# Performance work log

Hardware: AMD Instinct MI355X
Metric: run time of the kernel (lower is better)

The kernel has to match this reference:

```python
import jax, jax.numpy as jnp
import numpy as np

S, L = 512, 32            # number of sequences, max sequence length
IN_FEATURES = 13824       # 512*3*3 + 1024*3*3 ROI features
HID = 1024                # Head.hidden_dim
LSTM_H = HID // 2         # per-direction hidden size (bidirectional)
N_CLASSES = 4787
BN_EPS = 1e-5


def _make_ragged():
    lengths = (4 + (np.arange(S) % 29)).astype(np.int32)  # 4..32, sum = 9121
    n = int(lengths.sum())
    perm = np.random.RandomState(0).permutation(n).astype(np.int32)
    seq_idx = np.zeros((S, L), dtype=np.int32)
    off = 0
    for i, l in enumerate(lengths):
        seq_idx[i, :l] = perm[off:off + l]
        off += l
    return n, jnp.asarray(seq_idx), jnp.asarray(lengths)


def setup_inputs() -> dict:
    n, seq_idx, lengths = _make_ragged()
    key = jax.random.key(0)
    ks = jax.random.split(key, 16)
    w = lambda k, shp, s=0.02: (jax.random.normal(k, shp, dtype=jnp.float32) * s)
    return {
        "x": jax.random.normal(ks[0], (n, IN_FEATURES), dtype=jnp.float32),
        "fc1_w": w(ks[1], (HID, IN_FEATURES)),
        "fc1_b": w(ks[2], (HID,)),
        "bn_gamma": jnp.ones((HID,), jnp.float32),
        "bn_beta": jnp.zeros((HID,), jnp.float32),
        "fc2_w": w(ks[3], (N_CLASSES, HID)),
        "fc2_b": w(ks[4], (N_CLASSES,)),
        "w_ih_f": w(ks[5], (4 * LSTM_H, HID)),
        "w_hh_f": w(ks[6], (4 * LSTM_H, LSTM_H)),
        "b_ih_f": w(ks[7], (4 * LSTM_H,)),
        "b_hh_f": w(ks[8], (4 * LSTM_H,)),
        "w_ih_b": w(ks[9], (4 * LSTM_H, HID)),
        "w_hh_b": w(ks[10], (4 * LSTM_H, LSTM_H)),
        "b_ih_b": w(ks[11], (4 * LSTM_H,)),
        "b_hh_b": w(ks[12], (4 * LSTM_H,)),
        "seq_idx": seq_idx,
        "lengths": lengths,
    }


def _lstm_scan(seq_x, w_ih, w_hh, b_ih, b_hh):
    # seq_x: [S, L, HID] -> outputs [S, L, LSTM_H]; PyTorch gate order i,f,g,o
    s = seq_x.shape[0]
    h0 = jnp.zeros((s, LSTM_H), seq_x.dtype)
    c0 = jnp.zeros((s, LSTM_H), seq_x.dtype)
    x_gates = jnp.einsum('slh,gh->slg', seq_x, w_ih) + b_ih + b_hh  # precompute input gates

    def step(carry, xg):
        h, c = carry
        g = xg + h @ w_hh.T
        i, f, gg, o = jnp.split(g, 4, axis=-1)
        c = jax.nn.sigmoid(f) * c + jax.nn.sigmoid(i) * jnp.tanh(gg)
        h = jax.nn.sigmoid(o) * jnp.tanh(c)
        return (h, c), h

    _, hs = jax.lax.scan(step, (h0, c0), x_gates.transpose(1, 0, 2))  # [L, S, H]
    return hs.transpose(1, 0, 2)


def reference(x, fc1_w, fc1_b, bn_gamma, bn_beta, fc2_w, fc2_b,
              w_ih_f, w_hh_f, b_ih_f, b_hh_f,
              w_ih_b, w_hh_b, b_ih_b, b_hh_b,
              seq_idx, lengths):
    n = x.shape[0]
    # Head: fc1 -> relu -> BatchNorm1d (training-mode batch stats)
    h = jax.nn.relu(x @ fc1_w.T + fc1_b)
    mean = h.mean(axis=0)
    var = jnp.mean((h - mean) ** 2, axis=0)
    feats = (h - mean) * jax.lax.rsqrt(var + BN_EPS) * bn_gamma + bn_beta  # [N, HID]

    # ragged gather into packed [S, L, HID]
    mask = jnp.arange(L)[None, :] < lengths[:, None]          # [S, L]
    gidx = jnp.where(mask, seq_idx, 0)
    seq_x = feats[gidx] * mask[:, :, None]                    # zero padded slots

    # forward direction (padding at tail: harmless to causal scan)
    hf = _lstm_scan(seq_x, w_ih_f, w_hh_f, b_ih_f, b_hh_f)
    # backward direction: reverse each sequence within its valid length
    rev = jnp.clip(lengths[:, None] - 1 - jnp.arange(L)[None, :], 0, L - 1)  # [S, L]
    seq_rev = jnp.take_along_axis(seq_x, rev[:, :, None], axis=1)
    hb_rev = _lstm_scan(seq_rev, w_ih_b, w_hh_b, b_ih_b, b_hh_b)
    hb = jnp.take_along_axis(hb_rev, rev[:, :, None], axis=1)  # un-reverse (involution on valid region)

    out = jnp.concatenate([hf, hb], axis=-1)                   # [S, L, HID]

    # scatter back to flat roi order; padded slots dropped out-of-bounds
    sidx = jnp.where(mask, seq_idx, n).reshape(-1)
    lstm_feats = jnp.zeros((n, HID), feats.dtype).at[sidx].set(
        out.reshape(-1, HID), mode='drop')

    logits = lstm_feats @ fc2_w.T + fc2_b                      # apply_fc_out
    return logits
```

## Files before the change

kernel.cpp:

```cpp
#include <hip/hip_runtime.h>

typedef short short8v __attribute__((ext_vector_type(8)));
typedef float f32x4 __attribute__((ext_vector_type(4)));
typedef _Float16 h4v __attribute__((ext_vector_type(4)));

__device__ __forceinline__ unsigned short f2bf(float f){
  unsigned int u = __float_as_uint(f);
  u += 0x7fffu + ((u >> 16) & 1u);
  return (unsigned short)(u >> 16);
}
__device__ __forceinline__ float bf2f(unsigned short h){
  return __uint_as_float(((unsigned int)h) << 16);
}
union H2F { unsigned short u; _Float16 h; };
__device__ __forceinline__ float fp16f(unsigned short b){ H2F t; t.u = b; return (float)t.h; }

typedef __attribute__((address_space(1))) const unsigned int gu32;
typedef __attribute__((address_space(3))) unsigned int lu32;
__device__ __forceinline__ void gl16(const void* g, void* l){
  __builtin_amdgcn_global_load_lds((gu32*)g, (lu32*)l, 16, 0, 0);
}

template<int EPI>
__global__ __launch_bounds__(512, 2)
void gemm256(const unsigned short* __restrict__ A, const unsigned short* __restrict__ B,
             void* __restrict__ Cout, int M, int N, int K, int lda, int ldb, int ldc,
             const float* __restrict__ bias)
{
  __shared__ __align__(16) unsigned short As[2 * 2 * 256 * 32];
  __shared__ __align__(16) unsigned short Bs[2 * 2 * 256 * 32];

  const int tid = threadIdx.x;
  const int gx = gridDim.x;
  const int nwg = gx * gridDim.y;
  int dd = blockIdx.y * gx + blockIdx.x;
  int q8 = nwg >> 3, r8 = nwg & 7, xc = dd & 7, t8 = dd >> 3;
  int Lid = (xc < r8 ? xc * (q8 + 1) : r8 * (q8 + 1) + (xc - r8) * q8) + t8;
  const int bcol = (Lid % gx) * 256;
  const int brow = (Lid / gx) * 256;

  const int l = tid & 63, w = tid >> 6;
  const int wr = w >> 2;
  const int wn = w & 3;
  const int r16 = l & 15, kg = l >> 4;
  const int swz = (r16 >> 1) & 3;
  const int srow4 = l >> 2, sblk = l & 3;
  const int scol = (sblk ^ ((l >> 3) & 3)) * 8;

  const int kz = blockIdx.z * K;
  const unsigned short* Ag = A + (size_t)(brow + w * 32 + srow4) * lda + kz + scol;
  const unsigned short* Bg = B + (size_t)(bcol + w * 32 + srow4) * ldb + kz + scol;
  unsigned short* Asd = As + w * 1024;
  unsigned short* Bsd = Bs + w * 1024;

#define STA(buf, kh, kt) do { \
    gl16(Ag + (size_t)(kt) * 64 + (kh) * 32, Asd + (buf) * 16384 + (kh) * 8192); \
    gl16(Ag + (size_t)(kt) * 64 + (kh) * 32 + (size_t)16 * lda, Asd + (buf) * 16384 + (kh) * 8192 + 512); \
  } while (0)
#define STB(buf, kh, kt) do { \
    gl16(Bg + (size_t)(kt) * 64 + (kh) * 32, Bsd + (buf) * 16384 + (kh) * 8192); \
    gl16(Bg + (size_t)(kt) * 64 + (kh) * 32 + (size_t)16 * ldb, Bsd + (buf) * 16384 + (kh) * 8192 + 512); \
  } while (0)

  const unsigned short* Ard = As + (wr * 128 + r16) * 32 + ((kg ^ swz) * 8);
  const unsigned short* Brd = Bs + (wn * 64 + r16) * 32 + ((kg ^ swz) * 8);

  f32x4 acc[8][4];
  #pragma unroll
  for (int m = 0; m < 8; m++)
    #pragma unroll
    for (int nn = 0; nn < 4; nn++) { f32x4 z = {0.f, 0.f, 0.f, 0.f}; acc[m][nn] = z; }

  short8v af[4], bfr[4];

#define LDA4(c, kk, mq) { \
    _Pragma("unroll") for (int i = 0; i < 4; i++) \
      af[i] = *(const short8v*)(Ard + (c) * 16384 + (kk) * 8192 + ((mq) * 4 + i) * 512); }
#define LDB4(c, kk) { \
    _Pragma("unroll") for (int nn = 0; nn < 4; nn++) \
      bfr[nn] = *(const short8v*)(Brd + (c) * 16384 + (kk) * 8192 + nn * 512); }
#define MFMAQ(mq) { \
    __builtin_amdgcn_s_setprio(1); \
    _Pragma("unroll") for (int i = 0; i < 4; i++) { \
      _Pragma("unroll") for (int nn = 0; nn < 4; nn++) \
        acc[(mq) * 4 + i][nn] = __builtin_amdgcn_mfma_f32_16x16x32_bf16(af[i], bfr[nn], acc[(mq) * 4 + i][nn], 0, 0, 0); \
    } \
    __builtin_amdgcn_s_setprio(0); }

  const int nk = K >> 6;
  STA(0, 0, 0); STB(0, 0, 0); STA(0, 1, 0); STB(0, 1, 0);
  asm volatile("s_waitcnt vmcnt(4)" ::: "memory");
  __builtin_amdgcn_s_barrier();
  __builtin_amdgcn_sched_barrier(0);

  for (int j = 0; j < nk; j++) {
    const int c = j & 1, nb = c ^ 1;
    const bool pf = (j + 1 < nk);
    LDB4(c, 0); LDA4(c, 0, 0);
    if (pf) STA(nb, 0, j + 1);
    __builtin_amdgcn_s_barrier();
    MFMAQ(0);
    __builtin_amdgcn_s_barrier();
    LDA4(c, 0, 1);
    if (pf) STB(nb, 0, j + 1);
    __builtin_amdgcn_s_barrier();
    MFMAQ(1);
    if (pf) asm volatile("s_waitcnt vmcnt(4)" ::: "memory");
    else    asm volatile("s_waitcnt vmcnt(0)" ::: "memory");
    __builtin_amdgcn_s_barrier();
    __builtin_amdgcn_sched_barrier(0);
    LDB4(c, 1); LDA4(c, 1, 0);
    if (pf) STA(nb, 1, j + 1);
    __builtin_amdgcn_s_barrier();
    MFMAQ(0);
    __builtin_amdgcn_s_barrier();
    LDA4(c, 1, 1);
    if (pf) STB(nb, 1, j + 1);
    __builtin_amdgcn_s_barrier();
    MFMAQ(1);
    if (pf) asm volatile("s_waitcnt vmcnt(4)" ::: "memory");
    __builtin_amdgcn_s_barrier();
    __builtin_amdgcn_sched_barrier(0);
  }
#undef STA
#undef STB

  #pragma unroll
  for (int m = 0; m < 8; m++) {
    const int row0 = brow + wr * 128 + m * 16 + kg * 4;
    #pragma unroll
    for (int nn = 0; nn < 4; nn++) {
      const int col = bcol + wn * 64 + nn * 16 + r16;
      if (col < N) {
        const float bv = bias[col];
        #pragma unroll
        for (int rr = 0; rr < 4; rr++) {
          const int row = row0 + rr;
          if (row < M) {
            float val = acc[m][nn][rr] + bv;
            if (EPI == 3) {
              int dL = col >> 11, rc = col & 2047;
              int cg = rc >> 6, g = (rc >> 4) & 3, u = rc & 15;
              int pc = (dL << 11) + (((cg << 4) + u) << 2) + g;
              ((_Float16*)Cout)[(size_t)row * ldc + pc] = (_Float16)val;
            } else {
              ((float*)Cout)[(size_t)row * ldc + col] = val;
            }
          }
        }
      }
    }
  }
}

__global__ __launch_bounds__(512, 2)
void gemm256fA(const float* __restrict__ A, const unsigned short* __restrict__ B,
               _Float16* __restrict__ Cout, int M, int N, int K, int lda, int ldb, int ldc,
               int nvalid)
{
  __shared__ __align__(16) unsigned short As[2 * 2 * 256 * 32];
  __shared__ __align__(16) unsigned short Bs[2 * 2 * 256 * 32];

  const int tid = threadIdx.x;
  const int gx = gridDim.x;
  const int nwg = gx * gridDim.y;
  int dd = blockIdx.y * gx + blockIdx.x;
  int q8 = nwg >> 3, r8 = nwg & 7, xc = dd & 7, t8 = dd >> 3;
  int Lid = (xc < r8 ? xc * (q8 + 1) : r8 * (q8 + 1) + (xc - r8) * q8) + t8;
  const int bcol = (Lid % gx) * 256;
  const int brow = (Lid / gx) * 256;

  const int l = tid & 63, w = tid >> 6;
  const int wr = w >> 2;
  const int wn = w & 3;
  const int r16 = l & 15, kg = l >> 4;
  const int swz = (r16 >> 1) & 3;
  const int srow4 = l >> 2, sblk = l & 3;
  const int scol = (sblk ^ ((l >> 3) & 3)) * 8;

  const int kz = blockIdx.z * K;
  const unsigned short* Bg = B + (size_t)(bcol + w * 32 + srow4) * ldb + kz + scol;
  unsigned short* Bsd = Bs + w * 1024;

#define STB(buf, kh, kt) do { \
    gl16(Bg + (size_t)(kt) * 64 + (kh) * 32, Bsd + (buf) * 16384 + (kh) * 8192); \
    gl16(Bg + (size_t)(kt) * 64 + (kh) * 32 + (size_t)16 * ldb, Bsd + (buf) * 16384 + (kh) * 8192 + 512); \
  } while (0)

  const int rsel8 = l >> 3;
  const int g8 = l & 7;
  unsigned long long abase[4];
  int dstA[4];
  #pragma unroll
  for (int q = 0; q < 4; q++) {
    int row_local = w * 32 + q * 8 + rsel8;
    int rowA = brow + row_local;
    if (rowA >= nvalid) rowA = nvalid - 1;
    abase[q] = (unsigned long long)(A + (size_t)rowA * lda + kz + g8 * 8);
    int kh = g8 >> 2, gA = g8 & 3, swi = (row_local >> 1) & 3;
    dstA[q] = kh * 8192 + row_local * 32 + ((gA ^ swi) * 8);
  }

  const unsigned short* Ard = As + (wr * 128 + r16) * 32 + ((kg ^ swz) * 8);
  const unsigned short* Brd = Bs + (wn * 64 + r16) * 32 + ((kg ^ swz) * 8);

  f32x4 acc[8][4];
  #pragma unroll
  for (int m = 0; m < 8; m++)
    #pragma unroll
    for (int nn = 0; nn < 4; nn++) { f32x4 z = {0.f, 0.f, 0.f, 0.f}; acc[m][nn] = z; }

  short8v af[4], bfr[4];
  f32x4 ar[4][2];

#define ALOAD(kt) { \
    _Pragma("unroll") for (int q = 0; q < 4; q++) { \
      unsigned long long aq = abase[q] + (unsigned long long)(kt) * 256; \
      asm volatile("global_load_dwordx4 %0, %1, off" : "=v"(ar[q][0]) : "v"(aq) : "memory"); \
      asm volatile("global_load_dwordx4 %0, %1, off offset:16" : "=v"(ar[q][1]) : "v"(aq) : "memory"); \
    } }
#define AWRITE(buf) { \
    _Pragma("unroll") for (int q = 0; q < 4; q++) { \
      unsigned int d0_, d1_, d2_, d3_; \
      asm("v_cvt_pk_bf16_f32 %0, %1, %2" : "=v"(d0_) : "v"(ar[q][0][0]), "v"(ar[q][0][1])); \
      asm("v_cvt_pk_bf16_f32 %0, %1, %2" : "=v"(d1_) : "v"(ar[q][0][2]), "v"(ar[q][0][3])); \
      asm("v_cvt_pk_bf16_f32 %0, %1, %2" : "=v"(d2_) : "v"(ar[q][1][0]), "v"(ar[q][1][1])); \
      asm("v_cvt_pk_bf16_f32 %0, %1, %2" : "=v"(d3_) : "v"(ar[q][1][2]), "v"(ar[q][1][3])); \
      uint4 pv_; pv_.x = d0_; pv_.y = d1_; pv_.z = d2_; pv_.w = d3_; \
      *(uint4*)(As + (buf) * 16384 + dstA[q]) = pv_; \
    } }

  const int nk = K >> 6;
  ALOAD(0);
  STB(0, 0, 0); STB(0, 1, 0);
  asm volatile("s_waitcnt vmcnt(4)" ::: "memory");
  __builtin_amdgcn_sched_barrier(0);
  AWRITE(0);
  asm volatile("s_waitcnt vmcnt(0) lgkmcnt(0)" ::: "memory");
  __builtin_amdgcn_s_barrier();
  __builtin_amdgcn_sched_barrier(0);

#define LDA4(c, kk, mq) { \
    _Pragma("unroll") for (int i = 0; i < 4; i++) \
      af[i] = *(const short8v*)(Ard + (c) * 16384 + (kk) * 8192 + ((mq) * 4 + i) * 512); }
#define LDB4(c, kk) { \
    _Pragma("unroll") for (int nn = 0; nn < 4; nn++) \
      bfr[nn] = *(const short8v*)(Brd + (c) * 16384 + (kk) * 8192 + nn * 512); }
#define MFMAQ(mq) { \
    __builtin_amdgcn_s_setprio(1); \
    _Pragma("unroll") for (int i = 0; i < 4; i++) { \
      _Pragma("unroll") for (int nn = 0; nn < 4; nn++) \
        acc[(mq) * 4 + i][nn] = __builtin_amdgcn_mfma_f32_16x16x32_bf16(af[i], bfr[nn], acc[(mq) * 4 + i][nn], 0, 0, 0); \
    } \
    __builtin_amdgcn_s_setprio(0); }

  for (int j = 0; j < nk; j++) {
    const int c = j & 1, nb = c ^ 1;
    const bool pf = (j + 1 < nk);
    LDB4(c, 0); LDA4(c, 0, 0);
    if (pf) ALOAD(j + 1);
    __builtin_amdgcn_s_barrier();
    MFMAQ(0);
    __builtin_amdgcn_s_barrier();
    LDA4(c, 0, 1);
    if (pf) { STB(nb, 0, j + 1); STB(nb, 1, j + 1); }
    __builtin_amdgcn_s_barrier();
    MFMAQ(1);
    __builtin_amdgcn_s_barrier();
    __builtin_amdgcn_sched_barrier(0);
    LDB4(c, 1); LDA4(c, 1, 0);
    if (pf) {
      asm volatile("s_waitcnt vmcnt(4)" ::: "memory");
      __builtin_amdgcn_sched_barrier(0);
      AWRITE(nb);
    }
    __builtin_amdgcn_s_barrier();
    MFMAQ(0);
    __builtin_amdgcn_s_barrier();
    LDA4(c, 1, 1);
    __builtin_amdgcn_s_barrier();
    MFMAQ(1);
    asm volatile("s_waitcnt vmcnt(0) lgkmcnt(0)" ::: "memory");
    __builtin_amdgcn_s_barrier();
    __builtin_amdgcn_sched_barrier(0);
  }
#undef STB
#undef ALOAD
#undef AWRITE
#undef LDA4
#undef LDB4
#undef MFMAQ

  #pragma unroll
  for (int m = 0; m < 8; m++) {
    const int row0 = brow + wr * 128 + m * 16 + kg * 4;
    #pragma unroll
    for (int nn = 0; nn < 4; nn++) {
      const int col = bcol + wn * 64 + nn * 16 + r16;
      if (col < N) {
        #pragma unroll
        for (int rr = 0; rr < 4; rr++) {
          const int row = row0 + rr;
          if (row < M)
            Cout[(size_t)blockIdx.z * M * ldc + (size_t)row * ldc + col] = (_Float16)(acc[m][nn][rr]);
        }
      }
    }
  }
}

__global__ __launch_bounds__(256) void fc1_reduce(const _Float16* __restrict__ P, const float* __restrict__ bias,
                                                  unsigned short* __restrict__ h, float* __restrict__ part,
                                                  int n, int mpad) {
  int b = blockIdx.x, tid = threadIdx.x;
  int c0 = tid * 4;
  float4 bsv = *(const float4*)(bias + c0);
  float s[4] = {0,0,0,0}, qq[4] = {0,0,0,0};
  int rbeg = b * 32;
  for (int r = rbeg; r < rbeg + 32; r++) {
    h4v a0 = *(const h4v*)(P + (size_t)r * 1024 + c0);
    h4v a1 = *(const h4v*)(P + ((size_t)mpad + r) * 1024 + c0);
    h4v a2 = *(const h4v*)(P + ((size_t)2 * mpad + r) * 1024 + c0);
    float v0 = fmaxf((float)a0[0] + (float)a1[0] + (float)a2[0] + bsv.x, 0.f);
    float v1 = fmaxf((float)a0[1] + (float)a1[1] + (float)a2[1] + bsv.y, 0.f);
    float v2 = fmaxf((float)a0[2] + (float)a1[2] + (float)a2[2] + bsv.z, 0.f);
    float v3 = fmaxf((float)a0[3] + (float)a1[3] + (float)a2[3] + bsv.w, 0.f);
    if (r < n) {
      s[0] += v0; qq[0] += v0 * v0;
      s[1] += v1; qq[1] += v1 * v1;
      s[2] += v2; qq[2] += v2 * v2;
      s[3] += v3; qq[3] += v3 * v3;
    }
    *(ushort4*)(h + (size_t)r * 1024 + c0) = make_ushort4(f2bf(v0), f2bf(v1), f2bf(v2), f2bf(v3));
  }
  float* pp = part + (size_t)b * 2048;
  #pragma unroll
  for (int k = 0; k < 4; k++) { pp[(c0 + k) * 2] = s[k]; pp[(c0 + k) * 2 + 1] = qq[k]; }
}

__global__ __launch_bounds__(256, 1)
void lstm_persist(const unsigned short* __restrict__ whhc, const unsigned short* __restrict__ bcp,
                  const _Float16* __restrict__ G,
                  const int* __restrict__ gf, const int* __restrict__ gb, const int* __restrict__ sb,
                  unsigned short* __restrict__ hst,
                  unsigned short* __restrict__ lfeat, int* __restrict__ flags)
{
  __shared__ __align__(16) unsigned short Bsh[128 * 512];
  const int tid = threadIdx.x;
  const int l = tid & 63, w = tid >> 6;
  const int b = blockIdx.x;
  const int grp = b & 15;
  const int c = b >> 4;
  const int d = grp >> 3;
  const int rowbase = d * 512 + (grp & 7) * 64;
  const int r16 = l & 15, kg = l >> 4;
  const int swzl = (r16 & 7) * 8;
  const int hu0 = c * 32 + r16;

  const unsigned short* Bsrc = whhc + ((size_t)(d * 2048 + c * 128)) * 512;
  #pragma unroll
  for (int i = 0; i < 32; i++) {
    int rr = w * 32 + i;
    gl16(Bsrc + (size_t)rr * 512 + ((l * 8) ^ ((rr & 7) * 8)), Bsh + rr * 512);
  }
  asm volatile("s_waitcnt vmcnt(0)");
  __syncthreads();

  float creg[2][4];
  #pragma unroll
  for (int m = 0; m < 2; m++)
    #pragma unroll
    for (int rr = 0; rr < 4; rr++) creg[m][rr] = 0.f;

  const size_t stbase = (size_t)(((grp * 4 + w) * 16 + c) * 4 + (r16 >> 3)) * 128 + (size_t)kg * 32 + (r16 & 7);
  const size_t ldbase = ((size_t)(grp * 64 + w * 16) * 1024) + (size_t)l * 16;

  for (int t = 0; t < 32; t++) {
    ushort4 gv[2][4];
    int scv[4];
    #pragma unroll
    for (int rr = 0; rr < 4; rr++) {
      int row = rowbase + w * 16 + kg * 4 + rr;
      int sq = row & 511;
      int gi = d ? gb[sq * 32 + t] : gf[sq * 32 + t];
      const unsigned short* src = (gi >= 0)
          ? (const unsigned short*)G + ((size_t)gi * 4096 + (d << 11))
          : bcp + (d << 11);
      gv[0][rr] = *(const ushort4*)(src + hu0 * 4);
      gv[1][rr] = *(const ushort4*)(src + (hu0 + 16) * 4);
      scv[rr] = d ? sb[sq * 32 + t] : gi;
    }

    if (t > 0) {
      while (true) {
        int fv = 0x7fffffff;
        if (l < 16)
          fv = __hip_atomic_load(flags + ((grp * 16 + l) << 5), __ATOMIC_RELAXED, __HIP_MEMORY_SCOPE_AGENT);
        if (__all(fv >= t)) break;
        __builtin_amdgcn_s_sleep(1);
      }
    }
    asm volatile("" ::: "memory");

    const unsigned short* hp = hst + (size_t)(t & 1) * 524288;
    unsigned short* hn = hst + (size_t)((t + 1) & 1) * 524288;

    short8v av[16];
    {
      unsigned long long a64 = (unsigned long long)((const char*)hp + ldbase);
      #pragma unroll
      for (int kq = 0; kq < 4; kq++) {
        unsigned long long aq = a64 + (unsigned long long)kq * 4096;
        asm volatile("global_load_dwordx4 %0, %1, off offset:0 sc0 sc1"
                     : "=v"(av[kq * 4 + 0]) : "v"(aq) : "memory");
        asm volatile("global_load_dwordx4 %0, %1, off offset:1024 sc0 sc1"
                     : "=v"(av[kq * 4 + 1]) : "v"(aq) : "memory");
        asm volatile("global_load_dwordx4 %0, %1, off offset:2048 sc0 sc1"
                     : "=v"(av[kq * 4 + 2]) : "v"(aq) : "memory");
        asm volatile("global_load_dwordx4 %0, %1, off offset:3072 sc0 sc1"
                     : "=v"(av[kq * 4 + 3]) : "v"(aq) : "memory");
      }
    }
    asm volatile("s_waitcnt vmcnt(0)" ::: "memory");

    f32x4 acc[8];
    #pragma unroll
    for (int nn = 0; nn < 8; nn++) { f32x4 z = {0.f, 0.f, 0.f, 0.f}; acc[nn] = z; }

    #pragma unroll
    for (int kc = 0; kc < 8; kc++) {
      short8v bv[8][2];
      #pragma unroll
      for (int nn = 0; nn < 8; nn++)
        #pragma unroll
        for (int kk = 0; kk < 2; kk++)
          bv[nn][kk] = *(const short8v*)(Bsh + (nn * 16 + r16) * 512 + ((kc * 64 + kk * 32 + kg * 8) ^ swzl));
      #pragma unroll
      for (int kk = 0; kk < 2; kk++)
        #pragma unroll
        for (int nn = 0; nn < 8; nn++)
          acc[nn] = __builtin_amdgcn_mfma_f32_16x16x32_bf16(av[kc * 2 + kk], bv[nn][kk], acc[nn], 0, 0, 0);
    }

    unsigned long long ha = (unsigned long long)((char*)hn + stbase * 2);
    #pragma unroll
    for (int cgl = 0; cgl < 2; cgl++) {
      const int hu = hu0 + cgl * 16;
      #pragma unroll
      for (int reg = 0; reg < 4; reg++) {
        float g_i = acc[cgl * 4 + 0][reg] + fp16f(gv[cgl][reg].x);
        float g_f = acc[cgl * 4 + 1][reg] + fp16f(gv[cgl][reg].y);
        float g_g = acc[cgl * 4 + 2][reg] + fp16f(gv[cgl][reg].z);
        float g_o = acc[cgl * 4 + 3][reg] + fp16f(gv[cgl][reg].w);
        float si = 1.f / (1.f + __expf(-g_i));
        float sf = 1.f / (1.f + __expf(-g_f));
        float so = 1.f / (1.f + __expf(-g_o));
        float cn = sf * creg[cgl][reg] + si * tanhf(g_g);
        float hnv = so * tanhf(cn);
        creg[cgl][reg] = cn;
        unsigned int hb = f2bf(hnv);
        if (cgl == 0) {
          if (reg == 0) asm volatile("global_store_short %0, %1, off offset:0 sc0 sc1" :: "v"(ha), "v"(hb) : "memory");
          if (reg == 1) asm volatile("global_store_short %0, %1, off offset:16 sc0 sc1" :: "v"(ha), "v"(hb) : "memory");
          if (reg == 2) asm volatile("global_store_short %0, %1, off offset:32 sc0 sc1" :: "v"(ha), "v"(hb) : "memory");
          if (reg == 3) asm volatile("global_store_short %0, %1, off offset:48 sc0 sc1" :: "v"(ha), "v"(hb) : "memory");
        } else {
          if (reg == 0) asm volatile("global_store_short %0, %1, off offset:512 sc0 sc1" :: "v"(ha), "v"(hb) : "memory");
          if (reg == 1) asm volatile("global_store_short %0, %1, off offset:528 sc0 sc1" :: "v"(ha), "v"(hb) : "memory");
          if (reg == 2) asm volatile("global_store_short %0, %1, off offset:544 sc0 sc1" :: "v"(ha), "v"(hb) : "memory");
          if (reg == 3) asm volatile("global_store_short %0, %1, off offset:560 sc0 sc1" :: "v"(ha), "v"(hb) : "memory");
        }
        int sc = scv[reg];
        if (sc >= 0) lfeat[(size_t)sc * 1024 + d * 512 + hu] = f2bf(hnv);
      }
    }

    __syncthreads();
    if (t < 31 && tid == 0)
      __hip_atomic_store(flags + ((grp * 16 + c) << 5), t + 1, __ATOMIC_RELAXED, __HIP_MEMORY_SCOPE_AGENT);
  }
}

__global__ __launch_bounds__(256) void conv_bf16(const float* __restrict__ src, unsigned short* __restrict__ dst,
                                                 size_t nvalid, size_t total) {
  size_t stride = (size_t)gridDim.x * 2048;
  for (size_t i = ((size_t)blockIdx.x * 256 + threadIdx.x) * 8; i < total; i += stride) {
    unsigned short o[8];
    if (i + 8 <= nvalid) {
      float4 a = *(const float4*)(src + i);
      float4 b = *(const float4*)(src + i + 4);
      o[0] = f2bf(a.x); o[1] = f2bf(a.y); o[2] = f2bf(a.z); o[3] = f2bf(a.w);
      o[4] = f2bf(b.x); o[5] = f2bf(b.y); o[6] = f2bf(b.z); o[7] = f2bf(b.w);
    } else {
      #pragma unroll
      for (int j = 0; j < 8; j++) o[j] = (i + j < nvalid) ? f2bf(src[i + j]) : (unsigned short)0;
    }
    *(ushort4*)(dst + i) = make_ushort4(o[0], o[1], o[2], o[3]);
    *(ushort4*)(dst + i + 4) = make_ushort4(o[4], o[5], o[6], o[7]);
  }
}

__global__ __launch_bounds__(256) void bn_final(const float* __restrict__ part, const float* __restrict__ gamma,
                                                const float* __restrict__ beta, float* __restrict__ scale,
                                                float* __restrict__ shift, int M, int nb) {
  int c = blockIdx.x * 256 + threadIdx.x;
  float s = 0.f, q = 0.f;
  for (int b = 0; b < nb; b++) { s += part[(size_t)b * 2048 + c * 2]; q += part[(size_t)b * 2048 + c * 2 + 1]; }
  float mean = s / (float)M;
  float var = q / (float)M - mean * mean;
  float sc = gamma[c] * rsqrtf(var + 1e-5f);
  scale[c] = sc; shift[c] = beta[c] - mean * sc;
}

__global__ __launch_bounds__(256) void prep_tables(const int* __restrict__ seq_idx, const int* __restrict__ lengths,
                                                   int* __restrict__ gf, int* __restrict__ gb, int* __restrict__ sb) {
  int idx = blockIdx.x * 256 + threadIdx.x;
  if (idx < 512 * 32) {
    int s = idx >> 5, t = idx & 31;
    int len = lengths[s];
    gf[idx] = (t < len) ? seq_idx[idx] : -1;
    int rb = len - 1 - t;
    gb[idx] = seq_idx[(s << 5) + (rb < 0 ? 0 : rb)];
    sb[idx] = (t < len) ? seq_idx[(s << 5) + (len - 1 - t)] : -1;
  }
}

__global__ __launch_bounds__(256) void build_wih(const float* __restrict__ wf, const float* __restrict__ wb,
                                                 const float* __restrict__ bihf, const float* __restrict__ bhhf,
                                                 const float* __restrict__ bihb, const float* __restrict__ bhhb,
                                                 const float* __restrict__ scale, const float* __restrict__ shift,
                                                 unsigned short* __restrict__ wcdst, float* __restrict__ bc,
                                                 _Float16* __restrict__ bcp) {
  int orow = blockIdx.x * 4 + (threadIdx.x >> 6);
  int l = threadIdx.x & 63;
  int dir = orow >> 11, j = orow & 2047;
  int cc = j >> 6, jj = j & 63, g = jj >> 4, u = jj & 15;
  int srow = g * 512 + cc * 16 + u;
  const float* src = (dir ? wb : wf) + (size_t)srow * 1024;
  unsigned short* dst = wcdst + (size_t)orow * 1024;
  float sacc = 0.f;
  #pragma unroll
  for (int jv = 0; jv < 16; jv++) {
    int k = l + jv * 64;
    float v = src[k];
    sacc += shift[k] * v;
    dst[k] = f2bf(v * scale[k]);
  }
  #pragma unroll
  for (int o2 = 32; o2 > 0; o2 >>= 1) sacc += __shfl_down(sacc, o2);
  if (l == 0) {
    float bb = (dir ? (bihb[srow] + bhhb[srow]) : (bihf[srow] + bhhf[srow])) + sacc;
    bc[orow] = bb;
    int pc = (dir << 11) + (((cc << 4) + u) << 2) + g;
    bcp[pc] = (_Float16)bb;
  }
}

__global__ __launch_bounds__(256) void build_whh(const float* __restrict__ wf, const float* __restrict__ wb,
                                                 unsigned short* __restrict__ o) {
  int cidx = blockIdx.x * 256 + threadIdx.x;
  if (cidx < 4096 * 64) {
    int orow = cidx >> 6, k0 = (cidx & 63) * 8;
    int dir = orow >> 11, j = orow & 2047;
    int cc = j >> 7, L = j & 127;
    int cgl = L >> 6, g = (L >> 4) & 3, u = L & 15;
    int hunit = cc * 32 + cgl * 16 + u;
    const float* src = (dir ? wb : wf) + (size_t)(g * 512 + hunit) * 512 + k0;
    unsigned short* dst = o + (size_t)orow * 512 + k0;
    float4 a = *(const float4*)(src);
    float4 bq = *(const float4*)(src + 4);
    dst[0] = f2bf(a.x); dst[1] = f2bf(a.y); dst[2] = f2bf(a.z); dst[3] = f2bf(a.w);
    dst[4] = f2bf(bq.x); dst[5] = f2bf(bq.y); dst[6] = f2bf(bq.z); dst[7] = f2bf(bq.w);
  }
}

extern "C" void kernel_launch(void* const* d_in, const int* in_sizes, int n_in,
                              void* d_out, int out_size, void* d_ws, size_t ws_size,
                              hipStream_t stream) {
  const float* x     = (const float*)d_in[0];
  const float* fc1w  = (const float*)d_in[1];
  const float* fc1b  = (const float*)d_in[2];
  const float* gamma = (const float*)d_in[3];
  const float* beta  = (const float*)d_in[4];
  const float* fc2w  = (const float*)d_in[5];
  const float* fc2b  = (const float*)d_in[6];
  const float* wihf  = (const float*)d_in[7];
  const float* whhf  = (const float*)d_in[8];
  const float* bihf  = (const float*)d_in[9];
  const float* bhhf  = (const float*)d_in[10];
  const float* wihb  = (const float*)d_in[11];
  const float* whhb  = (const float*)d_in[12];
  const float* bihb  = (const float*)d_in[13];
  const float* bhhb  = (const float*)d_in[14];
  const int* seq_idx = (const int*)d_in[15];
  const int* lengths = (const int*)d_in[16];
  float* out = (float*)d_out;

  const int n = in_sizes[0] / 13824;
  const int mt = (n + 255) / 256;
  const int mpad = mt * 256;

  char* ws = (char*)d_ws;
  size_t off = 0;
  auto alloc = [&](size_t bytes) -> void* {
    void* p = ws + off; off += (bytes + 255) & ~(size_t)255; return p;
  };
  unsigned short* w1_h = (unsigned short*)alloc((size_t)1024 * 13824 * 2);
  unsigned short* w2_h = (unsigned short*)alloc((size_t)4864 * 1024 * 2);
  unsigned short* h    = (unsigned short*)alloc((size_t)mpad * 1024 * 2);
  _Float16*       G    = (_Float16*)alloc((size_t)mpad * 4096 * 2);
  unsigned short* wihc = (unsigned short*)alloc((size_t)4096 * 1024 * 2);
  unsigned short* whhc = (unsigned short*)alloc((size_t)4096 * 512 * 2);
  float* bias_c = (float*)alloc(4096 * 4);
  _Float16* bias_p = (_Float16*)alloc(4096 * 2);
  unsigned short* lfeat  = (unsigned short*)alloc((size_t)mpad * 1024 * 2);
  unsigned short* hstate = (unsigned short*)alloc((size_t)2 * 1024 * 512 * 2);
  float* part   = (float*)alloc((size_t)(mpad / 32) * 2048 * 4);
  float* scale  = (float*)alloc(1024 * 4);
  float* shift  = (float*)alloc(1024 * 4);
  int* gf  = (int*)alloc(16384 * 4);
  int* gb  = (int*)alloc(16384 * 4);
  int* sb  = (int*)alloc(16384 * 4);
  int* flags = (int*)alloc(256 * 32 * 4);

  _Float16* P16 = (_Float16*)G;

  dim3 blk(256);
  dim3 blk5(512);

  conv_bf16<<<1024, blk, 0, stream>>>(fc1w, w1_h, (size_t)1024 * 13824, (size_t)1024 * 13824);
  conv_bf16<<<256, blk, 0, stream>>>(fc2w, w2_h, (size_t)4787 * 1024, (size_t)4864 * 1024);
  build_whh<<<1024, blk, 0, stream>>>(whhf, whhb, whhc);
  prep_tables<<<64, blk, 0, stream>>>(seq_idx, lengths, gf, gb, sb);
  hipMemsetAsync(hstate, 0, (size_t)2 * 1024 * 512 * 2, stream);
  hipMemsetAsync(flags, 0, 256 * 32 * 4, stream);

  gemm256fA<<<dim3(4, mt, 3), blk5, 0, stream>>>(
      x, w1_h, P16, mpad, 1024, 4608, 13824, 13824, 1024, n);

  fc1_reduce<<<mpad / 32, blk, 0, stream>>>(P16, fc1b, h, part, n, mpad);
  bn_final<<<4, blk, 0, stream>>>(part, gamma, beta, scale, shift, n, mpad / 32);
  build_wih<<<1024, blk, 0, stream>>>(wihf, wihb, bihf, bhhf, bihb, bhhb, scale, shift, wihc, bias_c, bias_p);

  gemm256<3><<<dim3(16, mt), blk5, 0, stream>>>(
      h, wihc, G, n, 4096, 1024, 1024, 1024, 4096, bias_c);

  lstm_persist<<<256, blk, 0, stream>>>(whhc, (const unsigned short*)bias_p, G, gf, gb, sb,
                                        hstate, lfeat, flags);

  gemm256<0><<<dim3(19, mt), blk5, 0, stream>>>(
      lfeat, w2_h, out, n, 4787, 1024, 1024, 1024, 4787, fc2b);
}
```

Baseline: 1.091 ms.

## Shrink fc1 split-K GEMM tile to 128x128 with simpler pipeline and higher occupancy

Replaces the 256x256-tile fc1 GEMM (fp32 A converted to bf16 on the fly, split-K by 3) with a 128x128-tile variant. It uses a 64-wide K row with XOR swizzle, fewer barriers per iteration, and launch bounds allowing 4 blocks per CU. The grid grows to 8 x mpad/128 x 3, giving more workgroups for the 256 CUs. In exchange, each workgroup reuses data less, so traffic to global/L2 for the fp32 A matrix and the weights roughly doubles.

```diff
diff --git a/kernel.cpp b/kernel.cpp
--- a/kernel.cpp
+++ b/kernel.cpp
@@ -124,6 +124,9 @@
   }
 #undef STA
 #undef STB
+#undef LDA4
+#undef LDB4
+#undef MFMAQ
 
   #pragma unroll
   for (int m = 0; m < 8; m++) {
@@ -153,13 +156,13 @@
   }
 }
 
-__global__ __launch_bounds__(512, 2)
-void gemm256fA(const float* __restrict__ A, const unsigned short* __restrict__ B,
+__global__ __launch_bounds__(512, 4)
+void gemm128fA(const float* __restrict__ A, const unsigned short* __restrict__ B,
                _Float16* __restrict__ Cout, int M, int N, int K, int lda, int ldb, int ldc,
                int nvalid)
 {
-  __shared__ __align__(16) unsigned short As[2 * 2 * 256 * 32];
-  __shared__ __align__(16) unsigned short Bs[2 * 2 * 256 * 32];
+  __shared__ __align__(16) unsigned short As[2 * 128 * 64];
+  __shared__ __align__(16) unsigned short Bs[2 * 128 * 64];
 
   const int tid = threadIdx.x;
   const int gx = gridDim.x;
@@ -167,136 +170,115 @@
   int dd = blockIdx.y * gx + blockIdx.x;
   int q8 = nwg >> 3, r8 = nwg & 7, xc = dd & 7, t8 = dd >> 3;
   int Lid = (xc < r8 ? xc * (q8 + 1) : r8 * (q8 + 1) + (xc - r8) * q8) + t8;
-  const int bcol = (Lid % gx) * 256;
-  const int brow = (Lid / gx) * 256;
+  const int bcol = (Lid % gx) * 128;
+  const int brow = (Lid / gx) * 128;
 
   const int l = tid & 63, w = tid >> 6;
   const int wr = w >> 2;
   const int wn = w & 3;
   const int r16 = l & 15, kg = l >> 4;
-  const int swz = (r16 >> 1) & 3;
-  const int srow4 = l >> 2, sblk = l & 3;
-  const int scol = (sblk ^ ((l >> 3) & 3)) * 8;
+  const int swzl = (r16 & 7) * 8;
+  const int srow = l >> 3, sg = l & 7;
+  const int stg_off = (sg ^ srow) * 8;
 
   const int kz = blockIdx.z * K;
-  const unsigned short* Bg = B + (size_t)(bcol + w * 32 + srow4) * ldb + kz + scol;
-  unsigned short* Bsd = Bs + w * 1024;
-
-#define STB(buf, kh, kt) do { \
-    gl16(Bg + (size_t)(kt) * 64 + (kh) * 32, Bsd + (buf) * 16384 + (kh) * 8192); \
-    gl16(Bg + (size_t)(kt) * 64 + (kh) * 32 + (size_t)16 * ldb, Bsd + (buf) * 16384 + (kh) * 8192 + 512); \
+  const unsigned short* Bg = B + (size_t)bcol * ldb + kz + stg_off;
+
+#define STBK(buf, kt) do { \
+    gl16(Bg + (size_t)((w * 2 + 0) * 8 + srow) * ldb + (size_t)(kt) * 64, Bs + (buf) * 8192 + (w * 2 + 0) * 512); \
+    gl16(Bg + (size_t)((w * 2 + 1) * 8 + srow) * ldb + (size_t)(kt) * 64, Bs + (buf) * 8192 + (w * 2 + 1) * 512); \
   } while (0)
 
-  const int rsel8 = l >> 3;
-  const int g8 = l & 7;
-  unsigned long long abase[4];
-  int dstA[4];
-  #pragma unroll
-  for (int q = 0; q < 4; q++) {
-    int row_local = w * 32 + q * 8 + rsel8;
+  unsigned long long abase[2];
+  int dstA[2];
+  #pragma unroll
+  for (int q = 0; q < 2; q++) {
+    int row_local = w * 16 + q * 8 + srow;
     int rowA = brow + row_local;
     if (rowA >= nvalid) rowA = nvalid - 1;
-    abase[q] = (unsigned long long)(A + (size_t)rowA * lda + kz + g8 * 8);
-    int kh = g8 >> 2, gA = g8 & 3, swi = (row_local >> 1) & 3;
-    dstA[q] = kh * 8192 + row_local * 32 + ((gA ^ swi) * 8);
-  }
-
-  const unsigned short* Ard = As + (wr * 128 + r16) * 32 + ((kg ^ swz) * 8);
-  const unsigned short* Brd = Bs + (wn * 64 + r16) * 32 + ((kg ^ swz) * 8);
-
-  f32x4 acc[8][4];
-  #pragma unroll
-  for (int m = 0; m < 8; m++)
-    #pragma unroll
-    for (int nn = 0; nn < 4; nn++) { f32x4 z = {0.f, 0.f, 0.f, 0.f}; acc[m][nn] = z; }
-
-  short8v af[4], bfr[4];
-  f32x4 ar[4][2];
+    abase[q] = (unsigned long long)(A + (size_t)rowA * lda + kz + sg * 8);
+    dstA[q] = row_local * 64 + ((sg ^ srow) * 8);
+  }
+
+  const unsigned short* Ard = As + (wr * 64 + r16) * 64;
+  const unsigned short* Brd = Bs + (wn * 32 + r16) * 64;
+
+  f32x4 acc[4][2];
+  #pragma unroll
+  for (int m = 0; m < 4; m++)
+    #pragma unroll
+    for (int nn = 0; nn < 2; nn++) { f32x4 z = {0.f, 0.f, 0.f, 0.f}; acc[m][nn] = z; }
+
+  short8v af[4], bfr[2];
+  f32x4 ar[2][2];
 
 #define ALOAD(kt) { \
-    _Pragma("unroll") for (int q = 0; q < 4; q++) { \
+    _Pragma("unroll") for (int q = 0; q < 2; q++) { \
       unsigned long long aq = abase[q] + (unsigned long long)(kt) * 256; \
       asm volatile("global_load_dwordx4 %0, %1, off" : "=v"(ar[q][0]) : "v"(aq) : "memory"); \
       asm volatile("global_load_dwordx4 %0, %1, off offset:16" : "=v"(ar[q][1]) : "v"(aq) : "memory"); \
     } }
 #define AWRITE(buf) { \
-    _Pragma("unroll") for (int q = 0; q < 4; q++) { \
+    _Pragma("unroll") for (int q = 0; q < 2; q++) { \
       unsigned int d0_, d1_, d2_, d3_; \
       asm("v_cvt_pk_bf16_f32 %0, %1, %2" : "=v"(d0_) : "v"(ar[q][0][0]), "v"(ar[q][0][1])); \
       asm("v_cvt_pk_bf16_f32 %0, %1, %2" : "=v"(d1_) : "v"(ar[q][0][2]), "v"(ar[q][0][3])); \
       asm("v_cvt_pk_bf16_f32 %0, %1, %2" : "=v"(d2_) : "v"(ar[q][1][0]), "v"(ar[q][1][1])); \
       asm("v_cvt_pk_bf16_f32 %0, %1, %2" : "=v"(d3_) : "v"(ar[q][1][2]), "v"(ar[q][1][3])); \
       uint4 pv_; pv_.x = d0_; pv_.y = d1_; pv_.z = d2_; pv_.w = d3_; \
-      *(uint4*)(As + (buf) * 16384 + dstA[q]) = pv_; \
+      *(uint4*)(As + (buf) * 8192 + dstA[q]) = pv_; \
     } }
+#define LDAB(c, kk) { \
+    _Pragma("unroll") for (int i = 0; i < 4; i++) \
+      af[i] = *(const short8v*)(Ard + (c) * 8192 + i * 1024 + (((kk) * 32 + kg * 8) ^ swzl)); \
+    _Pragma("unroll") for (int nn = 0; nn < 2; nn++) \
+      bfr[nn] = *(const short8v*)(Brd + (c) * 8192 + nn * 1024 + (((kk) * 32 + kg * 8) ^ swzl)); }
+#define MFMA8() { \
+    __builtin_amdgcn_s_setprio(1); \
+    _Pragma("unroll") for (int i = 0; i < 4; i++) \
+      _Pragma("unroll") for (int nn = 0; nn < 2; nn++) \
+        acc[i][nn] = __builtin_amdgcn_mfma_f32_16x16x32_bf16(af[i], bfr[nn], acc[i][nn], 0, 0, 0); \
+    __builtin_amdgcn_s_setprio(0); }
 
   const int nk = K >> 6;
   ALOAD(0);
-  STB(0, 0, 0); STB(0, 1, 0);
-  asm volatile("s_waitcnt vmcnt(4)" ::: "memory");
+  STBK(0, 0);
+  asm volatile("s_waitcnt vmcnt(2)" ::: "memory");
   __builtin_amdgcn_sched_barrier(0);
   AWRITE(0);
   asm volatile("s_waitcnt vmcnt(0) lgkmcnt(0)" ::: "memory");
   __builtin_amdgcn_s_barrier();
   __builtin_amdgcn_sched_barrier(0);
 
-#define LDA4(c, kk, mq) { \
-    _Pragma("unroll") for (int i = 0; i < 4; i++) \
-      af[i] = *(const short8v*)(Ard + (c) * 16384 + (kk) * 8192 + ((mq) * 4 + i) * 512); }
-#define LDB4(c, kk) { \
-    _Pragma("unroll") for (int nn = 0; nn < 4; nn++) \
-      bfr[nn] = *(const short8v*)(Brd + (c) * 16384 + (kk) * 8192 + nn * 512); }
-#define MFMAQ(mq) { \
-    __builtin_amdgcn_s_setprio(1); \
-    _Pragma("unroll") for (int i = 0; i < 4; i++) { \
-      _Pragma("unroll") for (int nn = 0; nn < 4; nn++) \
-        acc[(mq) * 4 + i][nn] = __builtin_amdgcn_mfma_f32_16x16x32_bf16(af[i], bfr[nn], acc[(mq) * 4 + i][nn], 0, 0, 0); \
-    } \
-    __builtin_amdgcn_s_setprio(0); }
-
   for (int j = 0; j < nk; j++) {
     const int c = j & 1, nb = c ^ 1;
     const bool pf = (j + 1 < nk);
-    LDB4(c, 0); LDA4(c, 0, 0);
-    if (pf) ALOAD(j + 1);
-    __builtin_amdgcn_s_barrier();
-    MFMAQ(0);
-    __builtin_amdgcn_s_barrier();
-    LDA4(c, 0, 1);
-    if (pf) { STB(nb, 0, j + 1); STB(nb, 1, j + 1); }
-    __builtin_amdgcn_s_barrier();
-    MFMAQ(1);
-    __builtin_amdgcn_s_barrier();
-    __builtin_amdgcn_sched_barrier(0);
-    LDB4(c, 1); LDA4(c, 1, 0);
+    if (pf) { ALOAD(j + 1); STBK(nb, j + 1); }
+    LDAB(c, 0);
+    MFMA8();
+    LDAB(c, 1);
+    MFMA8();
     if (pf) {
-      asm volatile("s_waitcnt vmcnt(4)" ::: "memory");
+      asm volatile("s_waitcnt vmcnt(2)" ::: "memory");
       __builtin_amdgcn_sched_barrier(0);
       AWRITE(nb);
     }
-    __builtin_amdgcn_s_barrier();
-    MFMAQ(0);
-    __builtin_amdgcn_s_barrier();
-    LDA4(c, 1, 1);
-    __builtin_amdgcn_s_barrier();
-    MFMAQ(1);
     asm volatile("s_waitcnt vmcnt(0) lgkmcnt(0)" ::: "memory");
     __builtin_amdgcn_s_barrier();
     __builtin_amdgcn_sched_barrier(0);
   }
-#undef STB
+#undef STBK
 #undef ALOAD
 #undef AWRITE
-#undef LDA4
-#undef LDB4
-#undef MFMAQ
-
-  #pragma unroll
-  for (int m = 0; m < 8; m++) {
-    const int row0 = brow + wr * 128 + m * 16 + kg * 4;
-    #pragma unroll
-    for (int nn = 0; nn < 4; nn++) {
-      const int col = bcol + wn * 64 + nn * 16 + r16;
+#undef LDAB
+#undef MFMA8
+
+  #pragma unroll
+  for (int m = 0; m < 4; m++) {
+    const int row0 = brow + wr * 64 + m * 16 + kg * 4;
+    #pragma unroll
+    for (int nn = 0; nn < 2; nn++) {
+      const int col = bcol + wn * 32 + nn * 16 + r16;
       if (col < N) {
         #pragma unroll
         for (int rr = 0; rr < 4; rr++) {
@@ -599,6 +581,7 @@
   const int n = in_sizes[0] / 13824;
   const int mt = (n + 255) / 256;
   const int mpad = mt * 256;
+  const int mt128 = mpad / 128;
 
   char* ws = (char*)d_ws;
   size_t off = 0;
@@ -635,7 +618,7 @@
   hipMemsetAsync(hstate, 0, (size_t)2 * 1024 * 512 * 2, stream);
   hipMemsetAsync(flags, 0, 256 * 32 * 4, stream);
 
-  gemm256fA<<<dim3(4, mt, 3), blk5, 0, stream>>>(
+  gemm128fA<<<dim3(8, mt128, 3), blk5, 0, stream>>>(
       x, w1_h, P16, mpad, 1024, 4608, 13824, 13824, 1024, n);
 
   fc1_reduce<<<mpad / 32, blk, 0, stream>>>(P16, fc1b, h, part, n, mpad);
```

New measurement: 1.131 ms. +3.7%, slower.
